# Performance work log

Hardware: AMD Instinct MI355X
Metric: run time of the kernel (lower is better)

## Reference

```python
import jax, jax.numpy as jnp
import numpy as np

TEMPERATURE = 1.0

def _cauchy_kernel(x, y, temperature):
    # pairwise squared distances via Gram trick: ||x_i - y_j||^2
    sq_x = jnp.sum(x * x, axis=1)  # [n]
    sq_y = jnp.sum(y * y, axis=1)  # [m]
    d2 = sq_x[:, None] + sq_y[None, :] - 2.0 * (x @ y.T)
    d2 = jnp.maximum(d2, 0.0)
    return 1.0 / (1.0 + d2 / temperature)


def setup_inputs() -> dict:
    key = jax.random.key(0)
    k1, k2 = jax.random.split(key)
    features = jax.random.normal(k1, (8192, 128), dtype=jnp.float32)
    labels = jax.random.randint(k2, (8192,), 0, 1000, dtype=jnp.int64)
    return {"features": features, "labels": labels}


def reference(features, labels):
    b = features.shape[0] // 2
    z1 = features[:b]
    z2 = features[b:]
    z11 = _cauchy_kernel(z1, z1, TEMPERATURE)  # [b,b]
    z22 = _cauchy_kernel(z2, z2, TEMPERATURE)  # [b,b]
    z12 = _cauchy_kernel(z1, z2, TEMPERATURE)  # [b,b]

    eye = jnp.eye(b, dtype=z11.dtype)
    # positive term: mean log of matched-pair kernel (diagonal of z12)
    pos = jnp.sum(jnp.log(jnp.diagonal(z12))) / b
    # negative terms: row sums over [z11 - I | z12] and [z12^T | z22 - I]
    n1 = jnp.mean(jnp.log((z11 - eye).sum(axis=1) + z12.sum(axis=1)))
    n2 = jnp.mean(jnp.log(z12.sum(axis=0) + (z22 - eye).sum(axis=1)))
    neg = (n1 + n2) / 2.0
    return -(pos - neg)
```

## Files before the change

### kernel.cpp

```cpp
#include <hip/hip_runtime.h>
#include <math.h>

#define N_TOTAL 8192
#define BHALF   4096
#define KDIM    128
#define NTILE   64
#define NTRI    2080
#define NBLK_PW 512

typedef __bf16 bf16x8 __attribute__((ext_vector_type(8)));
typedef __bf16 bf16x2 __attribute__((ext_vector_type(2)));
typedef float  f32x4  __attribute__((ext_vector_type(4)));

#define GLOAD_LDS16(GSRC, LDST)                                                \
    __builtin_amdgcn_global_load_lds(                                          \
        (const __attribute__((address_space(1))) void*)(GSRC),                 \
        (__attribute__((address_space(3))) void*)(LDST), 16, 0, 0)

__global__ __launch_bounds__(256) void k_prep_pos(const float* __restrict__ F,
                                                  __bf16* __restrict__ Fbf,
                                                  float* __restrict__ sq,
                                                  float* __restrict__ posPart,
                                                  float* __restrict__ out) {
    int t = threadIdx.x;
    int w = t >> 6, l = t & 63;
    int p = blockIdx.x * 4 + w;
    const float2* r1 = (const float2*)(F + (size_t)p * KDIM);
    const float2* r2 = (const float2*)(F + (size_t)(p + BHALF) * KDIM);
    float2 a = r1[l];
    float2 c = r2[l];

    float s1 = fmaf(a.x, a.x, a.y * a.y);
    float s2 = fmaf(c.x, c.x, c.y * c.y);
    float dp = fmaf(a.x, c.x, a.y * c.y);
#pragma unroll
    for (int off = 32; off > 0; off >>= 1) {
        s1 += __shfl_down(s1, off);
        s2 += __shfl_down(s2, off);
        dp += __shfl_down(dp, off);
    }

    bf16x2 pa, pc;
    pa[0] = (__bf16)a.x; pa[1] = (__bf16)a.y;
    pc[0] = (__bf16)c.x; pc[1] = (__bf16)c.y;
    ((bf16x2*)(Fbf + (size_t)p * KDIM))[l] = pa;
    ((bf16x2*)(Fbf + (size_t)(p + BHALF) * KDIM))[l] = pc;

    __shared__ float posRed[4];
    if (l == 0) {
        sq[p] = s1;
        sq[p + BHALF] = s2;
        float d2 = fmaxf(s1 + s2 - 2.0f * dp, 0.0f);
        posRed[w] = logf(1.0f + d2);
    }
    __syncthreads();
    if (t == 0) {
        posPart[blockIdx.x] = posRed[0] + posRed[1] + posRed[2] + posRed[3];
        if (blockIdx.x == 0) out[0] = 0.0f;
    }
}

__global__ __launch_bounds__(512, 4) void k_pairwise(
        const __bf16* __restrict__ Fbf,
        const float* __restrict__ sq,
        float* __restrict__ Tpart) {
    __shared__ __align__(16) __bf16 As[128 * 128];
    __shared__ __align__(16) __bf16 Bs[128 * 128];
    __shared__ float rowAcc[128][2];
    __shared__ float colAcc[128][4];

    int t = threadIdx.x;
    int w = t >> 6;
    int l = t & 63;
    int wr = w >> 1, wc = w & 1;
    int low = l & 15, kb = l >> 4;

    int bid = blockIdx.x;
    int start = bid * 4 + (bid < 32 ? bid : 32);
    int cnt = (bid < 32) ? 5 : 4;

    int ti = (int)floorf((129.0f - sqrtf(16641.0f - 8.0f * (float)start)) * 0.5f);
    while (ti * (129 - ti) / 2 > start) --ti;
    while ((ti + 1) * (128 - ti) / 2 <= start) ++ti;
    int tj = ti + (start - ti * (129 - ti) / 2);

    int curTi = -1;
#pragma unroll 1
    for (int n = 0; n < cnt; ++n) {
        int I = ti * 128, J = tj * 128;
        bool diag = (ti == tj);

        if (ti != curTi) {
            const __bf16* FA = Fbf + (size_t)I * KDIM;
#pragma unroll
            for (int it = 0; it < 4; ++it) {
                int f = it * 512 + t;
                int row = f >> 4;
                int sg = f & 15;
                int g = sg ^ (row & 15);
                GLOAD_LDS16(FA + row * KDIM + g * 8, As + (size_t)f * 8);
            }
            curTi = ti;
        }
        if (!diag) {
            const __bf16* FB = Fbf + (size_t)J * KDIM;
#pragma unroll
            for (int it = 0; it < 4; ++it) {
                int f = it * 512 + t;
                int row = f >> 4;
                int sg = f & 15;
                int g = sg ^ (row & 15);
                GLOAD_LDS16(FB + row * KDIM + g * 8, Bs + (size_t)f * 8);
            }
        }
        __syncthreads();

        const bf16x8* Asg = (const bf16x8*)As;
        const bf16x8* Bsg = diag ? (const bf16x8*)As : (const bf16x8*)Bs;
        f32x4 acc[2][4] = {};
#pragma unroll
        for (int s = 0; s < 4; ++s) {
            int g = s * 4 + kb;
            bf16x8 aF[2], bF[4];
#pragma unroll
            for (int fr = 0; fr < 2; ++fr) {
                int R = wr * 32 + fr * 16 + low;
                aF[fr] = Asg[R * 16 + (g ^ low)];
            }
#pragma unroll
            for (int fc = 0; fc < 4; ++fc) {
                int C = wc * 64 + fc * 16 + low;
                bF[fc] = Bsg[C * 16 + (g ^ low)];
            }
#pragma unroll
            for (int fr = 0; fr < 2; ++fr)
#pragma unroll
                for (int fc = 0; fc < 4; ++fc)
                    acc[fr][fc] = __builtin_amdgcn_mfma_f32_16x16x32_bf16(
                        aF[fr], bF[fc], acc[fr][fc], 0, 0, 0);
        }

        float sqi[2][4], sqj[4];
#pragma unroll
        for (int fr = 0; fr < 2; ++fr)
#pragma unroll
            for (int r = 0; r < 4; ++r)
                sqi[fr][r] = sq[I + wr * 32 + fr * 16 + kb * 4 + r];
#pragma unroll
        for (int fc = 0; fc < 4; ++fc)
            sqj[fc] = sq[J + wc * 64 + fc * 16 + low];

        float rowPart[2][4] = {};
        float colPart[4] = {0.f, 0.f, 0.f, 0.f};
#pragma unroll
        for (int fr = 0; fr < 2; ++fr) {
#pragma unroll
            for (int fc = 0; fc < 4; ++fc) {
#pragma unroll
                for (int r = 0; r < 4; ++r) {
                    float d2 = sqi[fr][r] + sqj[fc] - 2.0f * acc[fr][fc][r];
                    d2 = fmaxf(d2, 0.0f);
                    float v = __builtin_amdgcn_rcpf(1.0f + d2);
                    rowPart[fr][r] += v;
                    colPart[fc] += v;
                }
            }
        }

#pragma unroll
        for (int fr = 0; fr < 2; ++fr)
#pragma unroll
            for (int r = 0; r < 4; ++r) {
                float x = rowPart[fr][r];
                x += __shfl_xor(x, 1);
                x += __shfl_xor(x, 2);
                x += __shfl_xor(x, 4);
                x += __shfl_xor(x, 8);
                if (low == 0)
                    rowAcc[wr * 32 + fr * 16 + kb * 4 + r][wc] = x;
            }

#pragma unroll
        for (int fc = 0; fc < 4; ++fc) {
            float x = colPart[fc];
            x += __shfl_xor(x, 16);
            x += __shfl_xor(x, 32);
            if (kb == 0)
                colAcc[wc * 64 + fc * 16 + low][wr] = x;
        }
        __syncthreads();

        if (t < 128) {
            Tpart[tj * N_TOTAL + I + t] = rowAcc[t][0] + rowAcc[t][1];
        } else if (t < 256 && !diag) {
            int c = t - 128;
            Tpart[ti * N_TOTAL + J + c] =
                colAcc[c][0] + colAcc[c][1] + colAcc[c][2] + colAcc[c][3];
        }

        ++tj;
        if (tj == NTILE) { ++ti; tj = ti; }
    }
}

__global__ __launch_bounds__(256) void k_final(const float* __restrict__ Tpart,
                                               const float* __restrict__ posPart,
                                               float* __restrict__ out) {
    int t = threadIdx.x;
    int i = blockIdx.x * 256 + t;
    float s = 0.0f;
#pragma unroll 8
    for (int k = 0; k < NTILE; ++k) s += Tpart[k * N_TOTAL + i];
    float v = logf(s - 1.0f);
    if (t < 32) v += 2.0f * posPart[blockIdx.x * 32 + t];
#pragma unroll
    for (int off = 32; off > 0; off >>= 1) v += __shfl_down(v, off);
    __shared__ float red[4];
    int w = t >> 6, l = t & 63;
    if (l == 0) red[w] = v;
    __syncthreads();
    if (t == 0) {
        float S = red[0] + red[1] + red[2] + red[3];
        atomicAdd(out, S * (1.0f / (2.0f * (float)BHALF)));
    }
}

extern "C" void kernel_launch(void* const* d_in, const int* in_sizes, int n_in,
                              void* d_out, int out_size, void* d_ws, size_t ws_size,
                              hipStream_t stream) {
    const float* F = (const float*)d_in[0];
    float* out = (float*)d_out;

    char* ws = (char*)d_ws;
    __bf16* Fbf    = (__bf16*)ws;
    float*  sq     = (float*)(ws + (size_t)N_TOTAL * KDIM * 2);
    float*  posPart = sq + N_TOTAL;
    float*  Tpart  = posPart + 1024;

    k_prep_pos<<<BHALF / 4, 256, 0, stream>>>(F, Fbf, sq, posPart, out);
    k_pairwise<<<NBLK_PW, 512, 0, stream>>>(Fbf, sq, Tpart);
    k_final<<<N_TOTAL / 256, 256, 0, stream>>>(Tpart, posPart, out);
}
```

Before: 85.65 us.

## Load MFMA fragments directly from global memory instead of staging through LDS

Removes the LDS staging of the A and B feature tiles. Each wave now reads its bf16x8 MFMA fragments straight from global memory (L2/L1-cached), which drops one __syncthreads per tile. The row and column reduction scratch is double-buffered by iteration parity so the next tile's writes cannot race with the previous tile's reads. In exchange the two wr waves sharing A rows and the four wc waves sharing B rows each re-read the same data from cache, and the vector loads are partly strided across rows.

Result: slower. 122.7 us (+43.3%).

```diff
diff --git a/kernel.cpp b/kernel.cpp
--- a/kernel.cpp
+++ b/kernel.cpp
@@ -5,17 +5,11 @@
 #define BHALF   4096
 #define KDIM    128
 #define NTILE   64
-#define NTRI    2080
-#define NBLK_PW 512
+#define NBLK    512
 
 typedef __bf16 bf16x8 __attribute__((ext_vector_type(8)));
 typedef __bf16 bf16x2 __attribute__((ext_vector_type(2)));
 typedef float  f32x4  __attribute__((ext_vector_type(4)));
-
-#define GLOAD_LDS16(GSRC, LDST)                                                \
-    __builtin_amdgcn_global_load_lds(                                          \
-        (const __attribute__((address_space(1))) void*)(GSRC),                 \
-        (__attribute__((address_space(3))) void*)(LDST), 16, 0, 0)
 
 __global__ __launch_bounds__(256) void k_prep_pos(const float* __restrict__ F,
                                                   __bf16* __restrict__ Fbf,
@@ -64,10 +58,8 @@
         const __bf16* __restrict__ Fbf,
         const float* __restrict__ sq,
         float* __restrict__ Tpart) {
-    __shared__ __align__(16) __bf16 As[128 * 128];
-    __shared__ __align__(16) __bf16 Bs[128 * 128];
-    __shared__ float rowAcc[128][2];
-    __shared__ float colAcc[128][4];
+    __shared__ float rowAcc[2][128][2];
+    __shared__ float colAcc[2][128][4];
 
     int t = threadIdx.x;
     int w = t >> 6;
@@ -84,54 +76,31 @@
     while ((ti + 1) * (128 - ti) / 2 <= start) ++ti;
     int tj = ti + (start - ti * (129 - ti) / 2);
 
-    int curTi = -1;
 #pragma unroll 1
     for (int n = 0; n < cnt; ++n) {
         int I = ti * 128, J = tj * 128;
         bool diag = (ti == tj);
-
-        if (ti != curTi) {
-            const __bf16* FA = Fbf + (size_t)I * KDIM;
-#pragma unroll
-            for (int it = 0; it < 4; ++it) {
-                int f = it * 512 + t;
-                int row = f >> 4;
-                int sg = f & 15;
-                int g = sg ^ (row & 15);
-                GLOAD_LDS16(FA + row * KDIM + g * 8, As + (size_t)f * 8);
-            }
-            curTi = ti;
-        }
-        if (!diag) {
-            const __bf16* FB = Fbf + (size_t)J * KDIM;
-#pragma unroll
-            for (int it = 0; it < 4; ++it) {
-                int f = it * 512 + t;
-                int row = f >> 4;
-                int sg = f & 15;
-                int g = sg ^ (row & 15);
-                GLOAD_LDS16(FB + row * KDIM + g * 8, Bs + (size_t)f * 8);
-            }
-        }
-        __syncthreads();
-
-        const bf16x8* Asg = (const bf16x8*)As;
-        const bf16x8* Bsg = diag ? (const bf16x8*)As : (const bf16x8*)Bs;
+        int buf = n & 1;
+
+        const __bf16* aP[2];
+        const __bf16* bP[4];
+#pragma unroll
+        for (int fr = 0; fr < 2; ++fr)
+            aP[fr] = Fbf + (size_t)(I + wr * 32 + fr * 16 + low) * KDIM + kb * 8;
+#pragma unroll
+        for (int fc = 0; fc < 4; ++fc)
+            bP[fc] = Fbf + (size_t)(J + wc * 64 + fc * 16 + low) * KDIM + kb * 8;
+
         f32x4 acc[2][4] = {};
 #pragma unroll
         for (int s = 0; s < 4; ++s) {
-            int g = s * 4 + kb;
             bf16x8 aF[2], bF[4];
 #pragma unroll
-            for (int fr = 0; fr < 2; ++fr) {
-                int R = wr * 32 + fr * 16 + low;
-                aF[fr] = Asg[R * 16 + (g ^ low)];
-            }
-#pragma unroll
-            for (int fc = 0; fc < 4; ++fc) {
-                int C = wc * 64 + fc * 16 + low;
-                bF[fc] = Bsg[C * 16 + (g ^ low)];
-            }
+            for (int fr = 0; fr < 2; ++fr)
+                aF[fr] = *(const bf16x8*)(aP[fr] + s * 32);
+#pragma unroll
+            for (int fc = 0; fc < 4; ++fc)
+                bF[fc] = *(const bf16x8*)(bP[fc] + s * 32);
 #pragma unroll
             for (int fr = 0; fr < 2; ++fr)
 #pragma unroll
@@ -177,7 +146,7 @@
                 x += __shfl_xor(x, 4);
                 x += __shfl_xor(x, 8);
                 if (low == 0)
-                    rowAcc[wr * 32 + fr * 16 + kb * 4 + r][wc] = x;
+                    rowAcc[buf][wr * 32 + fr * 16 + kb * 4 + r][wc] = x;
             }
 
 #pragma unroll
@@ -186,16 +155,16 @@
             x += __shfl_xor(x, 16);
             x += __shfl_xor(x, 32);
             if (kb == 0)
-                colAcc[wc * 64 + fc * 16 + low][wr] = x;
+                colAcc[buf][wc * 64 + fc * 16 + low][wr] = x;
         }
         __syncthreads();
 
         if (t < 128) {
-            Tpart[tj * N_TOTAL + I + t] = rowAcc[t][0] + rowAcc[t][1];
+            Tpart[tj * N_TOTAL + I + t] = rowAcc[buf][t][0] + rowAcc[buf][t][1];
         } else if (t < 256 && !diag) {
             int c = t - 128;
-            Tpart[ti * N_TOTAL + J + c] =
-                colAcc[c][0] + colAcc[c][1] + colAcc[c][2] + colAcc[c][3];
+            Tpart[ti * N_TOTAL + J + c] = colAcc[buf][c][0] + colAcc[buf][c][1] +
+                                          colAcc[buf][c][2] + colAcc[buf][c][3];
         }
 
         ++tj;
@@ -232,12 +201,12 @@
     float* out = (float*)d_out;
 
     char* ws = (char*)d_ws;
-    __bf16* Fbf    = (__bf16*)ws;
-    float*  sq     = (float*)(ws + (size_t)N_TOTAL * KDIM * 2);
+    __bf16* Fbf     = (__bf16*)ws;
+    float*  sq      = (float*)(ws + (size_t)N_TOTAL * KDIM * 2);
     float*  posPart = sq + N_TOTAL;
-    float*  Tpart  = posPart + 1024;
+    float*  Tpart   = posPart + 1024;
 
     k_prep_pos<<<BHALF / 4, 256, 0, stream>>>(F, Fbf, sq, posPart, out);
-    k_pairwise<<<NBLK_PW, 512, 0, stream>>>(Fbf, sq, Tpart);
+    k_pairwise<<<NBLK, 512, 0, stream>>>(Fbf, sq, Tpart);
     k_final<<<N_TOTAL / 256, 256, 0, stream>>>(Tpart, posPart, out);
 }
```
